# Kernel tuning notes

Hardware: AMD Instinct MI355X
Metric: run time of the kernel (lower is better)

Reference implementation:

```python
import jax, jax.numpy as jnp
import numpy as np

EPS = 1e-5
HEADS = 8
DIM_HEAD = 64
SCALE = DIM_HEAD ** -0.5
DEPTH = 4


def _layernorm(x, g, b):
    mu = jnp.mean(x, axis=-1, keepdims=True)
    var = jnp.var(x, axis=-1, keepdims=True)
    return (x - mu) * jax.lax.rsqrt(var + EPS) * g + b


def setup_inputs() -> dict:
    key = jax.random.key(0)
    ks = jax.random.split(key, 8)
    b, n, dim, mlp = 4, 1024, 512, 2048
    inner = HEADS * DIM_HEAD
    D = DEPTH
    s = 0.02  # realistic init scale
    return {
        "x": jax.random.normal(ks[0], (b, n, dim), jnp.float32),
        "ln1_g": jnp.ones((D, dim), jnp.float32),
        "ln1_b": jnp.zeros((D, dim), jnp.float32),
        "w_qkv": jax.random.normal(ks[1], (D, dim, 3 * inner), jnp.float32) * s,
        "reattn_w": jax.random.normal(ks[2], (D, HEADS, HEADS), jnp.float32),
        "rln_g": jnp.ones((D, HEADS), jnp.float32),
        "rln_b": jnp.zeros((D, HEADS), jnp.float32),
        "w_out": jax.random.normal(ks[3], (D, inner, dim), jnp.float32) * s,
        "b_out": jnp.zeros((D, dim), jnp.float32),
        "ln2_g": jnp.ones((D, dim), jnp.float32),
        "ln2_b": jnp.zeros((D, dim), jnp.float32),
        "w1": jax.random.normal(ks[4], (D, dim, mlp), jnp.float32) * s,
        "b1": jnp.zeros((D, mlp), jnp.float32),
        "w2": jax.random.normal(ks[5], (D, mlp, dim), jnp.float32) * s,
        "b2": jnp.zeros((D, dim), jnp.float32),
    }


def _attention(x, ln_g, ln_b, w_qkv, rw, rg, rb, w_out, b_out):
    b, n, dim = x.shape
    h, d = HEADS, DIM_HEAD
    hn = _layernorm(x, ln_g, ln_b)
    qkv = hn @ w_qkv  # [b, n, 3*h*d]
    q, k, v = jnp.split(qkv, 3, axis=-1)
    def to_heads(t):
        return t.reshape(b, n, h, d).transpose(0, 2, 1, 3)  # b h n d
    q, k, v = to_heads(q), to_heads(k), to_heads(v)
    dots = jnp.einsum('bhid,bhjd->bhij', q, k) * SCALE
    attn = jax.nn.softmax(dots, axis=-1)
    # cross-head re-attention mix
    attn = jnp.einsum('bhij,hg->bgij', attn, rw)
    # LayerNorm over the head axis (axis=1)
    mu = jnp.mean(attn, axis=1, keepdims=True)
    var = jnp.var(attn, axis=1, keepdims=True)
    attn = (attn - mu) * jax.lax.rsqrt(var + EPS)
    attn = attn * rg[None, :, None, None] + rb[None, :, None, None]
    out = jnp.einsum('bhij,bhjd->bhid', attn, v)
    out = out.transpose(0, 2, 1, 3).reshape(b, n, h * d)
    return out @ w_out + b_out


def _ffn(x, ln_g, ln_b, w1, b1, w2, b2):
    hn = _layernorm(x, ln_g, ln_b)
    hid = jax.nn.gelu(hn @ w1 + b1, approximate=False)
    return hid @ w2 + b2


def reference(x, ln1_g, ln1_b, w_qkv, reattn_w, rln_g, rln_b, w_out, b_out,
              ln2_g, ln2_b, w1, b1, w2, b2):
    for l in range(DEPTH):
        x = x + _attention(x, ln1_g[l], ln1_b[l], w_qkv[l], reattn_w[l],
                           rln_g[l], rln_b[l], w_out[l], b_out[l])
        x = x + _ffn(x, ln2_g[l], ln2_b[l], w1[l], b1[l], w2[l], b2[l])
        x = jnp.tanh(x)
    return x
```

## Files before the change

### kernel.cpp

```cpp
#include <hip/hip_runtime.h>
#include <math.h>

#define B 4
#define N 1024
#define DM 512
#define H 8
#define MLP 2048
#define TOK (B * N)
#define QKVW (3 * DM)
#define EPS 1e-5f
#define SCALE 0.125f

#define PS_HN  ((long)TOK * DM)
#define PS_WQ  ((long)QKVW * DM)

using short8 = __attribute__((ext_vector_type(8))) short;
using f32x4  = __attribute__((ext_vector_type(4))) float;
using u32x4  = __attribute__((ext_vector_type(4))) unsigned int;

__device__ __forceinline__ ushort f2b(float v) {
    unsigned int u = __builtin_bit_cast(unsigned int, v);
    u += 0x7fff + ((u >> 16) & 1);
    return (ushort)(u >> 16);
}
__device__ __forceinline__ float b2f(ushort u) {
    return __builtin_bit_cast(float, (unsigned int)u << 16);
}
__device__ __forceinline__ void split3(float v, ushort& h, ushort& l, ushort& q2) {
    h = f2b(v); float r1 = v - b2f(h);
    l = f2b(r1); q2 = f2b(r1 - b2f(l));
}
__device__ __forceinline__ void split_store8(f32x4 a0, f32x4 a1, char* base,
                                             int planeStride, int off) {
    short8 h8, l8, q8;
#pragma unroll
    for (int i = 0; i < 4; ++i) {
        ushort h, l, q;
        split3(a0[i], h, l, q);
        h8[i] = (short)h; l8[i] = (short)l; q8[i] = (short)q;
    }
#pragma unroll
    for (int i = 0; i < 4; ++i) {
        ushort h, l, q;
        split3(a1[i], h, l, q);
        h8[4 + i] = (short)h; l8[4 + i] = (short)l; q8[4 + i] = (short)q;
    }
    *(short8*)(base + off) = h8;
    *(short8*)(base + planeStride + off) = l8;
    *(short8*)(base + 2 * planeStride + off) = q8;
}

__global__ __launch_bounds__(256) void ln3_kernel(const float* __restrict__ x,
                                                  const float* __restrict__ g,
                                                  const float* __restrict__ bta,
                                                  ushort* __restrict__ out) {
    const int row = blockIdx.x;
    const int t = threadIdx.x;
    const float* xr = x + (size_t)row * DM;
    float v0 = xr[t], v1 = xr[t + 256];
    float s = v0 + v1, ss = v0 * v0 + v1 * v1;
    for (int o = 32; o; o >>= 1) {
        s += __shfl_down(s, o);
        ss += __shfl_down(ss, o);
    }
    __shared__ float ls[4], lss[4];
    const int wid = t >> 6, lane = t & 63;
    if (lane == 0) { ls[wid] = s; lss[wid] = ss; }
    __syncthreads();
    if (t == 0) {
        float S = ls[0] + ls[1] + ls[2] + ls[3];
        float SS = lss[0] + lss[1] + lss[2] + lss[3];
        float mu = S / DM;
        ls[0] = mu;
        lss[0] = SS / DM - mu * mu;
    }
    __syncthreads();
    const float mu = ls[0];
    const float r = rsqrtf(lss[0] + EPS);
    float o0 = (v0 - mu) * r * g[t] + bta[t];
    float o1 = (v1 - mu) * r * g[t + 256] + bta[t + 256];
    ushort h, l, q;
    size_t i0 = (size_t)row * DM + t;
    split3(o0, h, l, q);
    out[i0] = h; out[i0 + PS_HN] = l; out[i0 + 2 * PS_HN] = q;
    split3(o1, h, l, q);
    out[i0 + 256] = h; out[i0 + 256 + PS_HN] = l; out[i0 + 256 + 2 * PS_HN] = q;
}

template <int KS, bool TANH>
__global__ __launch_bounds__(256) void redln_kernel(
    const float* __restrict__ P, long pstride, const float* __restrict__ bias,
    const float* __restrict__ X, float* __restrict__ Xout,
    const float* __restrict__ g, const float* __restrict__ bta,
    ushort* __restrict__ out) {
    const int row = blockIdx.x;
    const int t = threadIdx.x;
    const size_t e0 = (size_t)row * DM + t;
    const size_t e1 = e0 + 256;
    float a0 = P[e0], a1 = P[e1];
#pragma unroll
    for (int k = 1; k < KS; ++k) {
        a0 += P[(size_t)k * pstride + e0];
        a1 += P[(size_t)k * pstride + e1];
    }
    float v0 = X[e0] + a0 + bias[t];
    float v1 = X[e1] + a1 + bias[t + 256];
    if (TANH) { v0 = tanhf(v0); v1 = tanhf(v1); }
    Xout[e0] = v0;
    Xout[e1] = v1;
    float s = v0 + v1, ss = v0 * v0 + v1 * v1;
    for (int o = 32; o; o >>= 1) {
        s += __shfl_down(s, o);
        ss += __shfl_down(ss, o);
    }
    __shared__ float ls[4], lss[4];
    const int wid = t >> 6, lane = t & 63;
    if (lane == 0) { ls[wid] = s; lss[wid] = ss; }
    __syncthreads();
    if (t == 0) {
        float S = ls[0] + ls[1] + ls[2] + ls[3];
        float SS = lss[0] + lss[1] + lss[2] + lss[3];
        float mu = S / DM;
        ls[0] = mu;
        lss[0] = SS / DM - mu * mu;
    }
    __syncthreads();
    const float mu = ls[0];
    const float r = rsqrtf(lss[0] + EPS);
    float o0 = (v0 - mu) * r * g[t] + bta[t];
    float o1 = (v1 - mu) * r * g[t + 256] + bta[t + 256];
    ushort h, l, q;
    split3(o0, h, l, q);
    out[e0] = h; out[e0 + PS_HN] = l; out[e0 + 2 * PS_HN] = q;
    split3(o1, h, l, q);
    out[e1] = h; out[e1 + PS_HN] = l; out[e1 + 2 * PS_HN] = q;
}

__global__ __launch_bounds__(256) void wtrans_kernel(const float* __restrict__ W,
                                                     ushort* __restrict__ WT,
                                                     int K, int Nn, long ps) {
    __shared__ float ts[32][33];
    const int n0 = blockIdx.x * 32, k0 = blockIdx.y * 32;
    const int tx = threadIdx.x & 31, ty = threadIdx.x >> 5;
#pragma unroll
    for (int p = 0; p < 4; ++p)
        ts[ty + p * 8][tx] = W[(size_t)(k0 + ty + p * 8) * Nn + n0 + tx];
    __syncthreads();
#pragma unroll
    for (int p = 0; p < 4; ++p) {
        float v = ts[tx][ty + p * 8];
        ushort h, l, q;
        split3(v, h, l, q);
        size_t idx = (size_t)(n0 + ty + p * 8) * K + k0 + tx;
        WT[idx] = h;
        WT[idx + ps] = l;
        WT[idx + 2 * ps] = q;
    }
}

__global__ __launch_bounds__(256) void vtrans_kernel(const float* __restrict__ v,
                                                     float* __restrict__ vt) {
    const int z = blockIdx.z, b = z >> 3, h = z & 7;
    __shared__ float ts[32][33];
    const int j0 = blockIdx.x * 32, d0 = blockIdx.y * 32;
    const int tx = threadIdx.x & 31, ty = threadIdx.x >> 5;
#pragma unroll
    for (int p = 0; p < 4; ++p)
        ts[ty + p * 8][tx] =
            v[(size_t)(b * N + j0 + ty + p * 8) * DM + h * 64 + d0 + tx];
    __syncthreads();
#pragma unroll
    for (int p = 0; p < 4; ++p)
        vt[(size_t)((b * H + h) * 64 + d0 + ty + p * 8) * N + j0 + tx] =
            ts[tx][ty + p * 8];
}

template <int BM, int BN, int WR, int WC, int EPI, bool AF32, bool BF32, int ZDIV>
__global__ __launch_bounds__(256) void mm3_kernel(
    const void* __restrict__ Av, int sA, long pA, long zA,
    const void* __restrict__ Bv, int sB, long pB, long zB,
    const float* __restrict__ bias, const float* __restrict__ res,
    void* __restrict__ Cv, int sC, long zC, long zCk, int K, float scale) {
    constexpr int WM = BM / WR, WN = BN / WC;
    constexpr int FM = WM / 16, FN = WN / 16;
    constexpr int RA = BM / 64, RB = BN / 64;
    static_assert(!AF32 || RA <= 2, "AF32 assumes BM<=128");
    static_assert(!BF32 || RB <= 2, "BF32 assumes BN<=128");
    int bx, by, z;
    {
        const int gx = gridDim.x, gy = gridDim.y;
        const long nwg = (long)gx * gy * gridDim.z;
        long o = ((long)blockIdx.z * gy + blockIdx.y) * gx + blockIdx.x;
        if ((nwg & 7) == 0) { const long q = nwg >> 3; o = (o & 7) * q + (o >> 3); }
        bx = (int)(o % gx);
        const long r1 = o / gx;
        by = (int)(r1 % gy);
        z  = (int)(r1 / gy);
    }
    const int zo = z / ZDIV, zk = z % ZDIV;
    const ushort* A  = AF32 ? nullptr : (const ushort*)Av + (size_t)zo * zA;
    const float*  Af = AF32 ? (const float*)Av + (size_t)zo * zA : nullptr;
    const ushort* Bt = BF32 ? nullptr : (const ushort*)Bv + (size_t)zo * zB;
    const float*  Bf = BF32 ? (const float*)Bv + (size_t)zo * zB : nullptr;
    __shared__ char lds[3 * (BM + BN) * 64];
    char* Bbase = lds + 3 * BM * 64;
    const int t = threadIdx.x;
    const int lane = t & 63, w = t >> 6;
    const int wr = w / WC, wc = w % WC;
    const int m0 = by * BM, n0 = bx * BN;
    const int sr = t >> 2, skg = t & 3;
    const int off0 = sr * 64 + 16 * (skg ^ ((sr >> 1) & 3));

    f32x4 acc[FM][FN];
#pragma unroll
    for (int i = 0; i < FM; ++i)
#pragma unroll
        for (int j = 0; j < FN; ++j) acc[i][j] = (f32x4){0.f, 0.f, 0.f, 0.f};

    u32x4 cA[3][RA], nA[3][RA], cB[3][RB], nB[3][RB];
    f32x4 cAf[2 * RA], nAf[2 * RA], cBf[2 * RB], nBf[2 * RB];

    auto loadAll = [&](int KT, u32x4 (&DA)[3][RA], f32x4 (&DAf)[2 * RA],
                       u32x4 (&DB)[3][RB], f32x4 (&DBf)[2 * RB]) {
        if constexpr (AF32) {
#pragma unroll
            for (int p = 0; p < RA; ++p) {
                const float* s_ = Af + (size_t)(m0 + sr + p * 64) * sA + KT + skg * 8;
                DAf[2 * p] = *(const f32x4*)s_;
                DAf[2 * p + 1] = *(const f32x4*)(s_ + 4);
            }
        } else {
#pragma unroll
            for (int pl = 0; pl < 3; ++pl)
#pragma unroll
                for (int p = 0; p < RA; ++p)
                    DA[pl][p] = *(const u32x4*)(A + (size_t)pl * pA +
                        (size_t)(m0 + sr + p * 64) * sA + KT + skg * 8);
        }
        if constexpr (BF32) {
#pragma unroll
            for (int p = 0; p < RB; ++p) {
                const float* s_ = Bf + (size_t)(n0 + sr + p * 64) * sB + KT + skg * 8;
                DBf[2 * p] = *(const f32x4*)s_;
                DBf[2 * p + 1] = *(const f32x4*)(s_ + 4);
            }
        } else {
#pragma unroll
            for (int pl = 0; pl < 3; ++pl)
#pragma unroll
                for (int p = 0; p < RB; ++p)
                    DB[pl][p] = *(const u32x4*)(Bt + (size_t)pl * pB +
                        (size_t)(n0 + sr + p * 64) * sB + KT + skg * 8);
        }
    };
    auto storeAll = [&](u32x4 (&DA)[3][RA], f32x4 (&DAf)[2 * RA],
                        u32x4 (&DB)[3][RB], f32x4 (&DBf)[2 * RB]) {
        if constexpr (AF32) {
#pragma unroll
            for (int p = 0; p < RA; ++p)
                split_store8(DAf[2 * p], DAf[2 * p + 1], lds, BM * 64,
                             p * 4096 + off0);
        } else {
#pragma unroll
            for (int pl = 0; pl < 3; ++pl)
#pragma unroll
                for (int p = 0; p < RA; ++p)
                    *(u32x4*)(lds + pl * BM * 64 + p * 4096 + off0) = DA[pl][p];
        }
        if constexpr (BF32) {
#pragma unroll
            for (int p = 0; p < RB; ++p)
                split_store8(DBf[2 * p], DBf[2 * p + 1], Bbase, BN * 64,
                             p * 4096 + off0);
        } else {
#pragma unroll
            for (int pl = 0; pl < 3; ++pl)
#pragma unroll
                for (int p = 0; p < RB; ++p)
                    *(u32x4*)(Bbase + pl * BN * 64 + p * 4096 + off0) = DB[pl][p];
        }
    };

    const int Kc = K / ZDIV;
    const int kbeg = zk * Kc;
    loadAll(kbeg, cA, cAf, cB, cBf);
    for (int kt = kbeg; kt < kbeg + Kc; kt += 32) {
        __syncthreads();
        storeAll(cA, cAf, cB, cBf);
        if (kt + 32 < kbeg + Kc) loadAll(kt + 32, nA, nAf, nB, nBf);
        __syncthreads();
        short8 af[3][FM], bf[3][FN];
        const int kg = lane >> 4;
#pragma unroll
        for (int pl = 0; pl < 3; ++pl)
#pragma unroll
            for (int i = 0; i < FM; ++i) {
                const int r = wr * WM + i * 16 + (lane & 15);
                af[pl][i] = *(const short8*)(lds + pl * BM * 64 + r * 64 +
                                             16 * (kg ^ ((r >> 1) & 3)));
            }
#pragma unroll
        for (int pl = 0; pl < 3; ++pl)
#pragma unroll
            for (int j = 0; j < FN; ++j) {
                const int r = wc * WN + j * 16 + (lane & 15);
                bf[pl][j] = *(const short8*)(Bbase + pl * BN * 64 + r * 64 +
                                             16 * (kg ^ ((r >> 1) & 3)));
            }
#pragma unroll
        for (int i = 0; i < FM; ++i)
#pragma unroll
            for (int j = 0; j < FN; ++j)
#pragma unroll
                for (int s = 2; s >= 0; --s)
#pragma unroll
                    for (int ph = 0; ph <= 2; ++ph) {
                        const int pb = s - ph;
                        if (pb < 0 || pb > 2) continue;
                        acc[i][j] = __builtin_amdgcn_mfma_f32_16x16x32_bf16(
                            af[ph][i], bf[pb][j], acc[i][j], 0, 0, 0);
                    }
        if constexpr (AF32) {
#pragma unroll
            for (int p = 0; p < 2 * RA; ++p) cAf[p] = nAf[p];
        } else {
#pragma unroll
            for (int pl = 0; pl < 3; ++pl)
#pragma unroll
                for (int p = 0; p < RA; ++p) cA[pl][p] = nA[pl][p];
        }
        if constexpr (BF32) {
#pragma unroll
            for (int p = 0; p < 2 * RB; ++p) cBf[p] = nBf[p];
        } else {
#pragma unroll
            for (int pl = 0; pl < 3; ++pl)
#pragma unroll
                for (int p = 0; p < RB; ++p) cB[pl][p] = nB[pl][p];
        }
    }
    float* Cbase = (float*)Cv + (size_t)zo * zC + (size_t)zk * zCk;
#pragma unroll
    for (int i = 0; i < FM; ++i) {
#pragma unroll
        for (int j = 0; j < FN; ++j) {
            const int col = n0 + wc * WN + j * 16 + (lane & 15);
#pragma unroll
            for (int r4 = 0; r4 < 4; ++r4) {
                const int row = m0 + wr * WM + i * 16 + (lane >> 4) * 4 + r4;
                float v = acc[i][j][r4];
                if (EPI == 1) v *= scale;
                if (EPI == 2) {
                    v += bias[col];
                    v = 0.5f * v * (1.0f + erff(v * 0.70710678118654752f));
                }
                if (EPI == 3) {
                    if (col < 1024)
                        ((float*)Cv)[(size_t)row * 1024 + col] = v;
                    else
                        const_cast<float*>(res)[(size_t)row * 512 + col - 1024] = v;
                } else {
                    Cbase[(size_t)row * sC + col] = v;
                }
            }
        }
    }
}

template <int KS, int MODE>
__global__ __launch_bounds__(256) void red_kernel(const float* __restrict__ P,
                                                  long pstride,
                                                  const float* __restrict__ bias,
                                                  const float* __restrict__ X,
                                                  float* __restrict__ out) {
    const size_t e = ((size_t)blockIdx.x * 256 + threadIdx.x) * 4;
    f32x4 a = *(const f32x4*)(P + e);
#pragma unroll
    for (int k = 1; k < KS; ++k) {
        f32x4 pk = *(const f32x4*)(P + (size_t)k * pstride + e);
#pragma unroll
        for (int i = 0; i < 4; ++i) a[i] += pk[i];
    }
    if (MODE >= 1) {
        f32x4 xb = *(const f32x4*)(X + e);
        f32x4 bb = *(const f32x4*)(bias + (e & (DM - 1)));
#pragma unroll
        for (int i = 0; i < 4; ++i) {
            float r = xb[i] + a[i] + bb[i];
            a[i] = (MODE == 2) ? tanhf(r) : r;
        }
    }
    *(f32x4*)(out + e) = a;
}

__global__ __launch_bounds__(256) void softmax_mix_kernel(float* __restrict__ d,
                                                          const float* __restrict__ rw,
                                                          const float* __restrict__ rg,
                                                          const float* __restrict__ rb) {
    const int i = blockIdx.x;
    const int t = threadIdx.x;
    const int lane = t & 63, wid = t >> 6;
    __shared__ float red[4];
    __shared__ float srw[64], srg[8], srb[8];
    if (t < 64) srw[t] = rw[t];
    if (t < 8) { srg[t] = rg[t]; srb[t] = rb[t]; }
    f32x4 p[8];
#pragma unroll
    for (int h = 0; h < 8; ++h) {
        p[h] = ((const f32x4*)(d + ((size_t)h * 1024 + i) * 1024))[t];
        float lm = fmaxf(fmaxf(p[h][0], p[h][1]), fmaxf(p[h][2], p[h][3]));
        for (int o = 32; o; o >>= 1) lm = fmaxf(lm, __shfl_down(lm, o));
        __syncthreads();
        if (lane == 0) red[wid] = lm;
        __syncthreads();
        const float M = fmaxf(fmaxf(red[0], red[1]), fmaxf(red[2], red[3]));
        float ls = 0.f;
#pragma unroll
        for (int u = 0; u < 4; ++u) {
            p[h][u] = expf(p[h][u] - M);
            ls += p[h][u];
        }
        for (int o = 32; o; o >>= 1) ls += __shfl_down(ls, o);
        __syncthreads();
        if (lane == 0) red[wid] = ls;
        __syncthreads();
        const float inv = 1.0f / (red[0] + red[1] + red[2] + red[3]);
#pragma unroll
        for (int u = 0; u < 4; ++u) p[h][u] *= inv;
    }
    f32x4 mg[8];
#pragma unroll
    for (int g = 0; g < 8; ++g) {
#pragma unroll
        for (int u = 0; u < 4; ++u) {
            float acc = 0.f;
#pragma unroll
            for (int h = 0; h < 8; ++h) acc += p[h][u] * srw[h * 8 + g];
            mg[g][u] = acc;
        }
    }
#pragma unroll
    for (int u = 0; u < 4; ++u) {
        float mean = 0.f;
#pragma unroll
        for (int g = 0; g < 8; ++g) mean += mg[g][u];
        mean *= 0.125f;
        float var = 0.f;
#pragma unroll
        for (int g = 0; g < 8; ++g) { float dd = mg[g][u] - mean; var += dd * dd; }
        var *= 0.125f;
        const float rs = rsqrtf(var + EPS);
#pragma unroll
        for (int g = 0; g < 8; ++g) mg[g][u] = (mg[g][u] - mean) * rs * srg[g] + srb[g];
    }
#pragma unroll
    for (int g = 0; g < 8; ++g)
        ((f32x4*)(d + ((size_t)g * 1024 + i) * 1024))[t] = mg[g];
}

extern "C" void kernel_launch(void* const* d_in, const int* in_sizes, int n_in,
                              void* d_out, int out_size, void* d_ws, size_t ws_size,
                              hipStream_t stream) {
    const float* x_in  = (const float*)d_in[0];
    const float* ln1_g = (const float*)d_in[1];
    const float* ln1_b = (const float*)d_in[2];
    const float* w_qkv = (const float*)d_in[3];
    const float* re_w  = (const float*)d_in[4];
    const float* rln_g = (const float*)d_in[5];
    const float* rln_b = (const float*)d_in[6];
    const float* w_out = (const float*)d_in[7];
    const float* b_out = (const float*)d_in[8];
    const float* ln2_g = (const float*)d_in[9];
    const float* ln2_b = (const float*)d_in[10];
    const float* w1    = (const float*)d_in[11];
    const float* b1    = (const float*)d_in[12];
    const float* w2    = (const float*)d_in[13];
    const float* b2    = (const float*)d_in[14];

    char* wsb = (char*)d_ws;
    float*  X    = (float*)wsb;
    float*  QKf  = (float*)(wsb + (8ull << 20));
    ushort* HN3f = (ushort*)(wsb + (8ull  << 20));
    float*  FPP  = (float*)(wsb + (8ull  << 20));
    ushort* W1T  = (ushort*)(wsb + (20ull << 20));
    float*  VTf  = (float*)(wsb + (24ull << 20));
    float*  D    = (float*)(wsb + (32ull << 20));
    float*  Vf   = (float*)(wsb + (32ull << 20));
    ushort* WOT  = (ushort*)(wsb + (32ull << 20));
    float*  OPP  = (float*)(wsb + (34ull << 20));
    ushort* W2T  = (ushort*)(wsb + (40ull << 20));
    ushort* WQT  = (ushort*)(wsb + (40ull << 20));
    ushort* HN3  = (ushort*)(wsb + (48ull << 20));
    float*  HIDf = (float*)(wsb + (48ull << 20));
    float*  AO   = (float*)(wsb + (64ull << 20));
    float*  PVP  = (float*)(wsb + (72ull << 20));

    hipMemcpyAsync(X, x_in, sizeof(float) * (size_t)TOK * DM,
                   hipMemcpyDeviceToDevice, stream);

    for (int l = 0; l < 4; ++l) {
        if (l == 0)
            ln3_kernel<<<TOK, 256, 0, stream>>>(X, ln1_g, ln1_b, HN3);
        wtrans_kernel<<<dim3(QKVW / 32, DM / 32), 256, 0, stream>>>(
            w_qkv + (size_t)l * DM * QKVW, WQT, DM, QKVW, PS_WQ);
        mm3_kernel<128, 128, 2, 2, 3, false, false, 1>
            <<<dim3(12, TOK / 128, 1), 256, 0, stream>>>(
            HN3, DM, PS_HN, 0, WQT, DM, PS_WQ, 0, nullptr, Vf,
            QKf, 1024, 0, 0, DM, 1.f);
        vtrans_kernel<<<dim3(N / 32, 2, B * H), 256, 0, stream>>>(Vf, VTf);

        for (int b = 0; b < B; ++b) {
            const float* qb = QKf + (size_t)b * N * 1024;
            mm3_kernel<64, 64, 2, 2, 1, true, true, 1>
                <<<dim3(16, 16, H), 256, 0, stream>>>(
                qb, 1024, 0, 64, qb + 512, 1024, 0, 64, nullptr, nullptr,
                D, 1024, (long)1024 * 1024, 0, 64, SCALE);
            softmax_mix_kernel<<<N, 256, 0, stream>>>(
                D, re_w + l * H * H, rln_g + l * H, rln_b + l * H);
            mm3_kernel<64, 64, 2, 2, 0, true, true, 4>
                <<<dim3(1, 16, H * 4), 256, 0, stream>>>(
                D, 1024, 0, (long)1024 * 1024,
                VTf + (size_t)b * H * 64 * N, 1024, 0, (long)64 * N,
                nullptr, nullptr,
                PVP, DM, 64, (long)N * DM, N, 1.f);
            red_kernel<4, 0><<<N * DM / 1024, 256, 0, stream>>>(
                PVP, (long)N * DM, nullptr, nullptr, AO + (size_t)b * N * DM);
        }
        wtrans_kernel<<<dim3(DM / 32, DM / 32), 256, 0, stream>>>(
            w_out + (size_t)l * DM * DM, WOT, DM, DM, (long)DM * DM);
        mm3_kernel<64, 128, 1, 4, 0, true, false, 2>
            <<<dim3(4, TOK / 64, 2), 256, 0, stream>>>(
            AO, DM, 0, 0, WOT, DM, (long)DM * DM, 0, nullptr, nullptr,
            OPP, DM, 0, (long)TOK * DM, DM, 1.f);
        redln_kernel<2, false><<<TOK, 256, 0, stream>>>(
            OPP, (long)TOK * DM, b_out + l * DM, X, X,
            ln2_g + l * DM, ln2_b + l * DM, HN3f);

        wtrans_kernel<<<dim3(MLP / 32, DM / 32), 256, 0, stream>>>(
            w1 + (size_t)l * DM * MLP, W1T, DM, MLP, (long)MLP * DM);
        mm3_kernel<128, 128, 2, 2, 2, false, false, 1>
            <<<dim3(MLP / 128, TOK / 128, 1), 256, 0, stream>>>(
            HN3f, DM, PS_HN, 0, W1T, DM, (long)MLP * DM, 0, b1 + l * MLP, nullptr,
            HIDf, MLP, 0, 0, DM, 1.f);
        wtrans_kernel<<<dim3(DM / 32, MLP / 32), 256, 0, stream>>>(
            w2 + (size_t)l * MLP * DM, W2T, MLP, DM, (long)DM * MLP);
        mm3_kernel<128, 128, 2, 2, 0, true, false, 4>
            <<<dim3(4, TOK / 128, 4), 256, 0, stream>>>(
            HIDf, MLP, 0, 0, W2T, MLP, (long)DM * MLP, 0, nullptr, nullptr,
            FPP, DM, 0, (long)TOK * DM, MLP, 1.f);
        if (l < 3) {
            redln_kernel<4, true><<<TOK, 256, 0, stream>>>(
                FPP, (long)TOK * DM, b2 + l * DM, X, X,
                ln1_g + (l + 1) * DM, ln1_b + (l + 1) * DM, HN3);
        } else {
            red_kernel<4, 2><<<TOK * DM / 1024, 256, 0, stream>>>(
                FPP, (long)TOK * DM, b2 + l * DM, X, (float*)d_out);
        }
    }
}
```

Baseline: 1.708 ms.

## Fuse PV split-K reduction into out-projection A-operand load

The attention PV matmul's split-K factor drops from 4 to 2. Its two partial outputs are written per batch into a full-token partial buffer, and the separate reduction kernel is removed. The out-projection GEMM gains an AKS template parameter that sums the split-K partials while loading its fp32 A operand. This cuts a kernel launch per batch and a read/write pass over the attention output. The cost is fewer workgroups in the PV GEMM and redundant partial-summing loads across out-projection column tiles.

```diff
diff --git a/kernel.cpp b/kernel.cpp
--- a/kernel.cpp
+++ b/kernel.cpp
@@ -175,17 +175,20 @@
             ts[tx][ty + p * 8];
 }
 
-template <int BM, int BN, int WR, int WC, int EPI, bool AF32, bool BF32, int ZDIV>
+template <int BM, int BN, int WR, int WC, int EPI, bool AF32, bool BF32,
+          int ZDIV, int AKS = 1>
 __global__ __launch_bounds__(256) void mm3_kernel(
     const void* __restrict__ Av, int sA, long pA, long zA,
     const void* __restrict__ Bv, int sB, long pB, long zB,
     const float* __restrict__ bias, const float* __restrict__ res,
-    void* __restrict__ Cv, int sC, long zC, long zCk, int K, float scale) {
+    void* __restrict__ Cv, int sC, long zC, long zCk, long aksA,
+    int K, float scale) {
     constexpr int WM = BM / WR, WN = BN / WC;
     constexpr int FM = WM / 16, FN = WN / 16;
     constexpr int RA = BM / 64, RB = BN / 64;
     static_assert(!AF32 || RA <= 2, "AF32 assumes BM<=128");
     static_assert(!BF32 || RB <= 2, "BF32 assumes BN<=128");
+    static_assert(AKS == 1 || AF32, "AKS>1 requires AF32");
     int bx, by, z;
     {
         const int gx = gridDim.x, gy = gridDim.y;
@@ -226,8 +229,18 @@
 #pragma unroll
             for (int p = 0; p < RA; ++p) {
                 const float* s_ = Af + (size_t)(m0 + sr + p * 64) * sA + KT + skg * 8;
-                DAf[2 * p] = *(const f32x4*)s_;
-                DAf[2 * p + 1] = *(const f32x4*)(s_ + 4);
+                f32x4 v0 = *(const f32x4*)s_;
+                f32x4 v1 = *(const f32x4*)(s_ + 4);
+#pragma unroll
+                for (int kk = 1; kk < AKS; ++kk) {
+                    const float* s2 = s_ + (size_t)kk * aksA;
+                    f32x4 w0 = *(const f32x4*)s2;
+                    f32x4 w1 = *(const f32x4*)(s2 + 4);
+#pragma unroll
+                    for (int i = 0; i < 4; ++i) { v0[i] += w0[i]; v1[i] += w1[i]; }
+                }
+                DAf[2 * p] = v0;
+                DAf[2 * p + 1] = v1;
             }
         } else {
 #pragma unroll
@@ -492,8 +505,7 @@
     ushort* WQT  = (ushort*)(wsb + (40ull << 20));
     ushort* HN3  = (ushort*)(wsb + (48ull << 20));
     float*  HIDf = (float*)(wsb + (48ull << 20));
-    float*  AO   = (float*)(wsb + (64ull << 20));
-    float*  PVP  = (float*)(wsb + (72ull << 20));
+    float*  PVP  = (float*)(wsb + (64ull << 20));
 
     hipMemcpyAsync(X, x_in, sizeof(float) * (size_t)TOK * DM,
                    hipMemcpyDeviceToDevice, stream);
@@ -506,7 +518,7 @@
         mm3_kernel<128, 128, 2, 2, 3, false, false, 1>
             <<<dim3(12, TOK / 128, 1), 256, 0, stream>>>(
             HN3, DM, PS_HN, 0, WQT, DM, PS_WQ, 0, nullptr, Vf,
-            QKf, 1024, 0, 0, DM, 1.f);
+            QKf, 1024, 0, 0, 0, DM, 1.f);
         vtrans_kernel<<<dim3(N / 32, 2, B * H), 256, 0, stream>>>(Vf, VTf);
 
         for (int b = 0; b < B; ++b) {
@@ -514,24 +526,22 @@
             mm3_kernel<64, 64, 2, 2, 1, true, true, 1>
                 <<<dim3(16, 16, H), 256, 0, stream>>>(
                 qb, 1024, 0, 64, qb + 512, 1024, 0, 64, nullptr, nullptr,
-                D, 1024, (long)1024 * 1024, 0, 64, SCALE);
+                D, 1024, (long)1024 * 1024, 0, 0, 64, SCALE);
             softmax_mix_kernel<<<N, 256, 0, stream>>>(
                 D, re_w + l * H * H, rln_g + l * H, rln_b + l * H);
-            mm3_kernel<64, 64, 2, 2, 0, true, true, 4>
-                <<<dim3(1, 16, H * 4), 256, 0, stream>>>(
+            mm3_kernel<64, 64, 2, 2, 0, true, true, 2>
+                <<<dim3(1, 16, H * 2), 256, 0, stream>>>(
                 D, 1024, 0, (long)1024 * 1024,
                 VTf + (size_t)b * H * 64 * N, 1024, 0, (long)64 * N,
                 nullptr, nullptr,
-                PVP, DM, 64, (long)N * DM, N, 1.f);
-            red_kernel<4, 0><<<N * DM / 1024, 256, 0, stream>>>(
-                PVP, (long)N * DM, nullptr, nullptr, AO + (size_t)b * N * DM);
+                PVP + (size_t)b * N * DM, DM, 64, (long)TOK * DM, 0, N, 1.f);
         }
         wtrans_kernel<<<dim3(DM / 32, DM / 32), 256, 0, stream>>>(
             w_out + (size_t)l * DM * DM, WOT, DM, DM, (long)DM * DM);
-        mm3_kernel<64, 128, 1, 4, 0, true, false, 2>
+        mm3_kernel<64, 128, 1, 4, 0, true, false, 2, 2>
             <<<dim3(4, TOK / 64, 2), 256, 0, stream>>>(
-            AO, DM, 0, 0, WOT, DM, (long)DM * DM, 0, nullptr, nullptr,
-            OPP, DM, 0, (long)TOK * DM, DM, 1.f);
+            PVP, DM, 0, 0, WOT, DM, (long)DM * DM, 0, nullptr, nullptr,
+            OPP, DM, 0, (long)TOK * DM, (long)TOK * DM, DM, 1.f);
         redln_kernel<2, false><<<TOK, 256, 0, stream>>>(
             OPP, (long)TOK * DM, b_out + l * DM, X, X,
             ln2_g + l * DM, ln2_b + l * DM, HN3f);
@@ -541,13 +551,13 @@
         mm3_kernel<128, 128, 2, 2, 2, false, false, 1>
             <<<dim3(MLP / 128, TOK / 128, 1), 256, 0, stream>>>(
             HN3f, DM, PS_HN, 0, W1T, DM, (long)MLP * DM, 0, b1 + l * MLP, nullptr,
-            HIDf, MLP, 0, 0, DM, 1.f);
+            HIDf, MLP, 0, 0, 0, DM, 1.f);
         wtrans_kernel<<<dim3(DM / 32, MLP / 32), 256, 0, stream>>>(
             w2 + (size_t)l * MLP * DM, W2T, MLP, DM, (long)DM * MLP);
         mm3_kernel<128, 128, 2, 2, 0, true, false, 4>
             <<<dim3(4, TOK / 128, 4), 256, 0, stream>>>(
             HIDf, MLP, 0, 0, W2T, MLP, (long)DM * MLP, 0, nullptr, nullptr,
-            FPP, DM, 0, (long)TOK * DM, MLP, 1.f);
+            FPP, DM, 0, (long)TOK * DM, 0, MLP, 1.f);
         if (l < 3) {
             redln_kernel<4, true><<<TOK, 256, 0, stream>>>(
                 FPP, (long)TOK * DM, b2 + l * DM, X, X,
```

New measurement: 1.744 ms. 1.02x slower.
